# Optimization experiments

Hardware: AMD Instinct MI355X
Metric: run time of the kernel (lower is better)

Reference implementation:

```python
import jax, jax.numpy as jnp
import numpy as np

EPS = 1e-8  # matches torch F.cosine_similarity eps default


def setup_inputs() -> dict:
    key = jax.random.key(0)
    k1, k2 = jax.random.split(key)
    z = jax.random.normal(k1, (8192, 256), dtype=jnp.float32)            # [N, d] node latents
    embedding_weight = jax.random.normal(k2, (4096, 256), dtype=jnp.float32)  # [V, d] codebook
    return {"z": z, "embedding_weight": embedding_weight}


def _l2_normalize(x):
    # torch cosine_similarity clamps each norm at eps before dividing
    n = jnp.sqrt(jnp.sum(x * x, axis=-1, keepdims=True))
    return x / jnp.maximum(n, EPS)


def reference(z, embedding_weight):
    # decode_edges: sigmoid(z @ z^T) -> [N, N]
    adj = jax.nn.sigmoid(jnp.matmul(z, z.T))

    # decode_node_features: cosine similarity of every node latent vs every
    # codebook vector, then argmax over the codebook axis. Instead of the
    # naive [N, V, d] broadcast, normalize both sides and take a single
    # [N, d] x [d, V] matmul -> [N, V], then reduce with argmax.
    zn = _l2_normalize(z)                   # [N, d]
    en = _l2_normalize(embedding_weight)    # [V, d]
    cosine_sim = jnp.matmul(zn, en.T)       # [N, V]
    decoded_indices = jnp.argmax(cosine_sim, axis=1)  # [N] int

    return adj, decoded_indices
```

## Files before the change

### kernel.cpp

```cpp
#include <hip/hip_runtime.h>
#include <stdint.h>
#include <math.h>

#define D_DIM 256
#define NZ 8192
#define NV 4096

typedef __bf16 bf16;
typedef __attribute__((ext_vector_type(8))) __bf16 bf16x8;
typedef __attribute__((ext_vector_type(4))) float f32x4;

__device__ __forceinline__ void stage16(const bf16* g, bf16* lbase) {
#if __has_builtin(__builtin_amdgcn_global_load_lds)
  __builtin_amdgcn_global_load_lds(
      (const __attribute__((address_space(1))) void*)(uintptr_t)g,
      (__attribute__((address_space(3))) void*)(uint32_t)(uintptr_t)lbase,
      16, 0, 0);
#endif
}

__global__ void prep_kernel(const float* __restrict__ z, const float* __restrict__ E,
                            bf16* __restrict__ zh, bf16* __restrict__ zl,
                            bf16* __restrict__ eh, float* __restrict__ rinvZ,
                            float* __restrict__ rinvE,
                            unsigned long long* __restrict__ slots) {
  __shared__ float red[4];
  const int row = blockIdx.x;
  const int t = threadIdx.x;
  const bool isZ = row < NZ;
  const int r = isZ ? row : row - NZ;
  const float* src = isZ ? z : E;
  const float x = src[(size_t)r * D_DIM + t];
  const bf16 h = (bf16)x;
  if (isZ) {
    zh[(size_t)r * D_DIM + t] = h;
    zl[(size_t)r * D_DIM + t] = (bf16)(x - (float)h);
  } else {
    eh[(size_t)r * D_DIM + t] = h;
  }
  float s = x * x;
#pragma unroll
  for (int off = 32; off; off >>= 1) s += __shfl_xor(s, off);
  if ((t & 63) == 0) red[t >> 6] = s;
  __syncthreads();
  if (t == 0) {
    const float tot = red[0] + red[1] + red[2] + red[3];
    const float rv = 1.0f / fmaxf(sqrtf(tot), 1e-8f);
    if (isZ) {
      rinvZ[r] = rv;
      slots[r] = 0ull;
    } else {
      rinvE[r] = rv;
    }
  }
}

__device__ __forceinline__ unsigned long long packvc(float v, int col) {
  const uint32_t b = __float_as_uint(v);
  const uint32_t key = b ^ ((uint32_t)((int32_t)b >> 31) | 0x80000000u);
  return ((unsigned long long)key << 32) | (uint32_t)(~(uint32_t)col);
}

__global__ __launch_bounds__(256, 2) void cos_kernel(
    const bf16* __restrict__ Ah, const bf16* __restrict__ Bh, bf16* __restrict__ Dm,
    const float* __restrict__ rinvZ, const float* __restrict__ rinvE,
    unsigned long long* __restrict__ slots) {
  __shared__ bf16 lAh[128 * 32], lBh[128 * 32];
  const int tid = threadIdx.x;
  const int lane = tid & 63;
  const int w = tid >> 6;
  const int wr = w >> 1, wc = w & 1;
  const int l15 = lane & 15, q = lane >> 4;
  const int bm = blockIdx.y * 128;
  const int bn = blockIdx.x * 128;

  f32x4 acc[4][4] = {};

  for (int kt = 0; kt < 8; ++kt) {
    const int ko = kt * 32;
#pragma unroll
    for (int i = 0; i < 2; ++i) {
      const int c = w * 128 + i * 64 + lane;
      const int r = c >> 2;
      const int kb = (c & 3) << 3;
      const int lofs = (w * 128 + i * 64) * 8;
      stage16(Ah + (size_t)(bm + r) * D_DIM + ko + kb, lAh + lofs);
      stage16(Bh + (size_t)(bn + r) * D_DIM + ko + kb, lBh + lofs);
    }
    __syncthreads();
    bf16x8 fa[4], fb[4];
#pragma unroll
    for (int ms = 0; ms < 4; ++ms)
      fa[ms] = *(const bf16x8*)&lAh[(wr * 64 + ms * 16 + l15) * 32 + q * 8];
#pragma unroll
    for (int ns = 0; ns < 4; ++ns)
      fb[ns] = *(const bf16x8*)&lBh[(wc * 64 + ns * 16 + l15) * 32 + q * 8];
#pragma unroll
    for (int ms = 0; ms < 4; ++ms)
#pragma unroll
      for (int ns = 0; ns < 4; ++ns)
        acc[ms][ns] = __builtin_amdgcn_mfma_f32_16x16x32_bf16(fa[ms], fb[ns], acc[ms][ns], 0, 0, 0);
    __syncthreads();
  }

  float rc[4];
  int cols[4];
#pragma unroll
  for (int ns = 0; ns < 4; ++ns) {
    cols[ns] = bn + wc * 64 + ns * 16 + l15;
    rc[ns] = rinvE[cols[ns]];
  }
#pragma unroll
  for (int ms = 0; ms < 4; ++ms) {
    const int rb = bm + wr * 64 + ms * 16 + q * 4;
#pragma unroll
    for (int r = 0; r < 4; ++r) {
      const int rowg = rb + r;
      const float rr = rinvZ[rowg];
      bf16* drow = Dm + (size_t)rowg * NV;
      unsigned long long best = 0ull;
#pragma unroll
      for (int ns = 0; ns < 4; ++ns) {
        const float v = acc[ms][ns][r] * rc[ns] * rr;
        drow[cols[ns]] = (bf16)v;
        const unsigned long long p = packvc(v, cols[ns]);
        best = p > best ? p : best;
      }
#pragma unroll
      for (int off = 1; off < 16; off <<= 1) {
        const unsigned long long o = __shfl_xor(best, off);
        best = o > best ? o : best;
      }
      if (l15 == 0) atomicMax(&slots[rowg], best);
    }
  }
}

__device__ __forceinline__ int tri_base(int i) { return i * 64 - ((i * (i - 1)) >> 1); }

__global__ __launch_bounds__(256, 2) void adj_kernel(const bf16* __restrict__ Ah,
                                                     const bf16* __restrict__ Al,
                                                     float* __restrict__ out) {
  __shared__ bf16 lAh[128 * 32], lAl[128 * 32], lBh[128 * 32], lBl[128 * 32];
  int k = blockIdx.x;
  k = (k & 7) * 260 + (k >> 3);
  const double disc = 4160.25 - 2.0 * (double)k;
  int bi = (int)(64.5 - sqrt(disc));
  while (tri_base(bi + 1) <= k) ++bi;
  while (tri_base(bi) > k) --bi;
  const int bj = bi + (k - tri_base(bi));
  const int bm = bi * 128, bn = bj * 128;

  const int tid = threadIdx.x;
  const int lane = tid & 63;
  const int w = tid >> 6;
  const int wr = w >> 1, wc = w & 1;
  const int l15 = lane & 15, q = lane >> 4;

  f32x4 acc[4][4] = {};

  for (int kt = 0; kt < 8; ++kt) {
    const int ko = kt * 32;
#pragma unroll
    for (int i = 0; i < 2; ++i) {
      const int c = w * 128 + i * 64 + lane;
      const int r = c >> 2;
      const int kb = (c & 3) << 3;
      const size_t ga = (size_t)(bm + r) * D_DIM + ko + kb;
      const size_t gb = (size_t)(bn + r) * D_DIM + ko + kb;
      const int lofs = (w * 128 + i * 64) * 8;
      stage16(Ah + ga, lAh + lofs);
      stage16(Al + ga, lAl + lofs);
      stage16(Ah + gb, lBh + lofs);
      stage16(Al + gb, lBl + lofs);
    }
    __syncthreads();
    bf16x8 fah[4], fal[4], fbh[4], fbl[4];
#pragma unroll
    for (int ms = 0; ms < 4; ++ms) {
      const int m = wr * 64 + ms * 16 + l15;
      fah[ms] = *(const bf16x8*)&lAh[m * 32 + q * 8];
      fal[ms] = *(const bf16x8*)&lAl[m * 32 + q * 8];
    }
#pragma unroll
    for (int ns = 0; ns < 4; ++ns) {
      const int n = wc * 64 + ns * 16 + l15;
      fbh[ns] = *(const bf16x8*)&lBh[n * 32 + q * 8];
      fbl[ns] = *(const bf16x8*)&lBl[n * 32 + q * 8];
    }
#pragma unroll
    for (int ms = 0; ms < 4; ++ms)
#pragma unroll
      for (int ns = 0; ns < 4; ++ns) {
        acc[ms][ns] = __builtin_amdgcn_mfma_f32_16x16x32_bf16(fah[ms], fbh[ns], acc[ms][ns], 0, 0, 0);
        acc[ms][ns] = __builtin_amdgcn_mfma_f32_16x16x32_bf16(fah[ms], fbl[ns], acc[ms][ns], 0, 0, 0);
        acc[ms][ns] = __builtin_amdgcn_mfma_f32_16x16x32_bf16(fal[ms], fbh[ns], acc[ms][ns], 0, 0, 0);
      }
    __syncthreads();
  }

#pragma unroll
  for (int ms = 0; ms < 4; ++ms)
#pragma unroll
    for (int ns = 0; ns < 4; ++ns)
#pragma unroll
      for (int r = 0; r < 4; ++r)
        acc[ms][ns][r] = __builtin_amdgcn_rcpf(1.0f + __expf(-acc[ms][ns][r]));

#pragma unroll
  for (int ms = 0; ms < 4; ++ms) {
    const int rb = bm + wr * 64 + ms * 16 + q * 4;
#pragma unroll
    for (int r = 0; r < 4; ++r) {
      const size_t ro = (size_t)(rb + r) * NZ;
#pragma unroll
      for (int ns = 0; ns < 4; ++ns) {
        const int col = bn + wc * 64 + ns * 16 + l15;
        out[ro + col] = acc[ms][ns][r];
      }
    }
  }
  if (bi != bj) {
#pragma unroll
    for (int ms = 0; ms < 4; ++ms) {
      const int rb = bm + wr * 64 + ms * 16 + q * 4;
#pragma unroll
      for (int ns = 0; ns < 4; ++ns) {
        const int col = bn + wc * 64 + ns * 16 + l15;
        *(f32x4*)&out[(size_t)col * NZ + rb] = acc[ms][ns];
      }
    }
  }
}

__device__ __forceinline__ double block_reduce(double v, double* red, int t) {
#pragma unroll
  for (int off = 32; off; off >>= 1) v += __shfl_xor(v, off);
  __syncthreads();
  if ((t & 63) == 0) red[t >> 6] = v;
  __syncthreads();
  return red[0] + red[1] + red[2] + red[3];
}

__global__ __launch_bounds__(256) void refine_kernel(
    const bf16* __restrict__ Dm, const unsigned long long* __restrict__ slots,
    const float* __restrict__ z, const float* __restrict__ E,
    float* __restrict__ out_idx) {
  __shared__ int s_cand[128];
  __shared__ int s_cnt;
  __shared__ double s_red[4];
  const int row = blockIdx.x;
  const int t = threadIdx.x;
  if (t == 0) s_cnt = 0;
  __syncthreads();

  const unsigned long long packed = slots[row];
  const uint32_t key = (uint32_t)(packed >> 32);
  const uint32_t fb = (key & 0x80000000u) ? (key ^ 0x80000000u) : ~key;
  const float M = __uint_as_float(fb);
  const float thr = M - 2e-2f;

  const bf16* drow = Dm + (size_t)row * NV;
  for (int c8 = t; c8 < NV / 8; c8 += 256) {
    const bf16x8 v = *(const bf16x8*)(drow + c8 * 8);
#pragma unroll
    for (int j = 0; j < 8; ++j) {
      if ((float)v[j] >= thr) {
        const int kk = atomicAdd(&s_cnt, 1);
        if (kk < 128) s_cand[kk] = c8 * 8 + j;
      }
    }
  }
  __syncthreads();
  const int cnt = s_cnt < 128 ? s_cnt : 128;

  const double zv = (double)z[(size_t)row * D_DIM + t];
  const double sz2 = block_reduce(zv * zv, s_red, t);

  double v1 = -1e30, v2 = -1e30;
  int c1 = 0x7fffffff, c2 = 0x7fffffff;
  for (int i = 0; i < cnt; ++i) {
    const int c = s_cand[i];
    const double ev = (double)E[(size_t)c * D_DIM + t];
    const double dot = block_reduce(zv * ev, s_red, t);
    const double se2 = block_reduce(ev * ev, s_red, t);
    if (t == 0) {
      const double cv = dot / (fmax(sqrt(sz2), 1e-8) * fmax(sqrt(se2), 1e-8));
      if (cv > v1 || (cv == v1 && c < c1)) {
        v2 = v1; c2 = c1; v1 = cv; c1 = c;
      } else if (cv > v2 || (cv == v2 && c < c2)) {
        v2 = cv; c2 = c;
      }
    }
  }
  if (t == 0) {
    int pick = c1;
    if (c2 != 0x7fffffff && (v1 - v2) < 3e-7) pick = c2;
    out_idx[row] = (float)pick;
  }
}

extern "C" void kernel_launch(void* const* d_in, const int* in_sizes, int n_in,
                              void* d_out, int out_size, void* d_ws, size_t ws_size,
                              hipStream_t stream) {
  const float* z = (const float*)d_in[0];
  const float* E = (const float*)d_in[1];
  float* out = (float*)d_out;

  char* ws = (char*)d_ws;
  bf16* zh = (bf16*)ws;
  bf16* zl = zh + (size_t)NZ * D_DIM;
  bf16* eh = zl + (size_t)NZ * D_DIM;
  float* rinvZ = (float*)(eh + (size_t)NV * D_DIM);
  float* rinvE = rinvZ + NZ;
  unsigned long long* slots = (unsigned long long*)(rinvE + NV);

  bf16* Dm = (bf16*)out;
  float* idx_out = out + (size_t)NZ * NZ;

  prep_kernel<<<NZ + NV, 256, 0, stream>>>(z, E, zh, zl, eh, rinvZ, rinvE, slots);

  dim3 g2(NV / 128, NZ / 128);
  cos_kernel<<<g2, 256, 0, stream>>>(zh, eh, Dm, rinvZ, rinvE, slots);

  refine_kernel<<<NZ, 256, 0, stream>>>(Dm, slots, z, E, idx_out);

  adj_kernel<<<2080, 256, 0, stream>>>(zh, zl, out);
}
```

Baseline: 434.2 us.

## Parallelize refine candidates across waves and raise GEMM occupancy to three blocks

The refine kernel now scores candidates with one wave each, using shuffle reductions, instead of running two block-wide reductions with barriers per candidate. It also narrows the candidate threshold, which cuts how many candidates get rescored. Both GEMM kernels now load A fragments per row-subtile inside the loop, which lowers register pressure, and their launch bounds rise to three blocks per SIMD to allow more occupancy. The tighter threshold risks missing the true argmax when bf16 rounding error is large, and the new launch bound may cause register spills.

After: 393.9 us. -9.3%, faster.

```diff
diff --git a/kernel.cpp b/kernel.cpp
--- a/kernel.cpp
+++ b/kernel.cpp
@@ -61,7 +61,7 @@
   return ((unsigned long long)key << 32) | (uint32_t)(~(uint32_t)col);
 }
 
-__global__ __launch_bounds__(256, 2) void cos_kernel(
+__global__ __launch_bounds__(256, 3) void cos_kernel(
     const bf16* __restrict__ Ah, const bf16* __restrict__ Bh, bf16* __restrict__ Dm,
     const float* __restrict__ rinvZ, const float* __restrict__ rinvE,
     unsigned long long* __restrict__ slots) {
@@ -88,18 +88,17 @@
       stage16(Bh + (size_t)(bn + r) * D_DIM + ko + kb, lBh + lofs);
     }
     __syncthreads();
-    bf16x8 fa[4], fb[4];
-#pragma unroll
-    for (int ms = 0; ms < 4; ++ms)
-      fa[ms] = *(const bf16x8*)&lAh[(wr * 64 + ms * 16 + l15) * 32 + q * 8];
+    bf16x8 fb[4];
 #pragma unroll
     for (int ns = 0; ns < 4; ++ns)
       fb[ns] = *(const bf16x8*)&lBh[(wc * 64 + ns * 16 + l15) * 32 + q * 8];
 #pragma unroll
-    for (int ms = 0; ms < 4; ++ms)
+    for (int ms = 0; ms < 4; ++ms) {
+      const bf16x8 fa = *(const bf16x8*)&lAh[(wr * 64 + ms * 16 + l15) * 32 + q * 8];
 #pragma unroll
       for (int ns = 0; ns < 4; ++ns)
-        acc[ms][ns] = __builtin_amdgcn_mfma_f32_16x16x32_bf16(fa[ms], fb[ns], acc[ms][ns], 0, 0, 0);
+        acc[ms][ns] = __builtin_amdgcn_mfma_f32_16x16x32_bf16(fa, fb[ns], acc[ms][ns], 0, 0, 0);
+    }
     __syncthreads();
   }
 
@@ -138,7 +137,7 @@
 
 __device__ __forceinline__ int tri_base(int i) { return i * 64 - ((i * (i - 1)) >> 1); }
 
-__global__ __launch_bounds__(256, 2) void adj_kernel(const bf16* __restrict__ Ah,
+__global__ __launch_bounds__(256, 3) void adj_kernel(const bf16* __restrict__ Ah,
                                                      const bf16* __restrict__ Al,
                                                      float* __restrict__ out) {
   __shared__ bf16 lAh[128 * 32], lAl[128 * 32], lBh[128 * 32], lBl[128 * 32];
@@ -175,13 +174,7 @@
       stage16(Al + gb, lBl + lofs);
     }
     __syncthreads();
-    bf16x8 fah[4], fal[4], fbh[4], fbl[4];
-#pragma unroll
-    for (int ms = 0; ms < 4; ++ms) {
-      const int m = wr * 64 + ms * 16 + l15;
-      fah[ms] = *(const bf16x8*)&lAh[m * 32 + q * 8];
-      fal[ms] = *(const bf16x8*)&lAl[m * 32 + q * 8];
-    }
+    bf16x8 fbh[4], fbl[4];
 #pragma unroll
     for (int ns = 0; ns < 4; ++ns) {
       const int n = wc * 64 + ns * 16 + l15;
@@ -189,13 +182,17 @@
       fbl[ns] = *(const bf16x8*)&lBl[n * 32 + q * 8];
     }
 #pragma unroll
-    for (int ms = 0; ms < 4; ++ms)
+    for (int ms = 0; ms < 4; ++ms) {
+      const int m = wr * 64 + ms * 16 + l15;
+      const bf16x8 fah = *(const bf16x8*)&lAh[m * 32 + q * 8];
+      const bf16x8 fal = *(const bf16x8*)&lAl[m * 32 + q * 8];
 #pragma unroll
       for (int ns = 0; ns < 4; ++ns) {
-        acc[ms][ns] = __builtin_amdgcn_mfma_f32_16x16x32_bf16(fah[ms], fbh[ns], acc[ms][ns], 0, 0, 0);
-        acc[ms][ns] = __builtin_amdgcn_mfma_f32_16x16x32_bf16(fah[ms], fbl[ns], acc[ms][ns], 0, 0, 0);
-        acc[ms][ns] = __builtin_amdgcn_mfma_f32_16x16x32_bf16(fal[ms], fbh[ns], acc[ms][ns], 0, 0, 0);
-      }
+        acc[ms][ns] = __builtin_amdgcn_mfma_f32_16x16x32_bf16(fah, fbh[ns], acc[ms][ns], 0, 0, 0);
+        acc[ms][ns] = __builtin_amdgcn_mfma_f32_16x16x32_bf16(fah, fbl[ns], acc[ms][ns], 0, 0, 0);
+        acc[ms][ns] = __builtin_amdgcn_mfma_f32_16x16x32_bf16(fal, fbh[ns], acc[ms][ns], 0, 0, 0);
+      }
+    }
     __syncthreads();
   }
 
@@ -231,15 +228,6 @@
       }
     }
   }
-}
-
-__device__ __forceinline__ double block_reduce(double v, double* red, int t) {
-#pragma unroll
-  for (int off = 32; off; off >>= 1) v += __shfl_xor(v, off);
-  __syncthreads();
-  if ((t & 63) == 0) red[t >> 6] = v;
-  __syncthreads();
-  return red[0] + red[1] + red[2] + red[3];
 }
 
 __global__ __launch_bounds__(256) void refine_kernel(
@@ -248,9 +236,13 @@
     float* __restrict__ out_idx) {
   __shared__ int s_cand[128];
   __shared__ int s_cnt;
-  __shared__ double s_red[4];
+  __shared__ double s_dot[128];
+  __shared__ double s_se2[128];
+  __shared__ double s_sz2;
   const int row = blockIdx.x;
   const int t = threadIdx.x;
+  const int lane = t & 63;
+  const int w = t >> 6;
   if (t == 0) s_cnt = 0;
   __syncthreads();
 
@@ -258,7 +250,7 @@
   const uint32_t key = (uint32_t)(packed >> 32);
   const uint32_t fb = (key & 0x80000000u) ? (key ^ 0x80000000u) : ~key;
   const float M = __uint_as_float(fb);
-  const float thr = M - 2e-2f;
+  const float thr = M - 1.2e-2f;
 
   const bf16* drow = Dm + (size_t)row * NV;
   for (int c8 = t; c8 < NV / 8; c8 += 256) {
@@ -274,26 +266,51 @@
   __syncthreads();
   const int cnt = s_cnt < 128 ? s_cnt : 128;
 
-  const double zv = (double)z[(size_t)row * D_DIM + t];
-  const double sz2 = block_reduce(zv * zv, s_red, t);
-
-  double v1 = -1e30, v2 = -1e30;
-  int c1 = 0x7fffffff, c2 = 0x7fffffff;
-  for (int i = 0; i < cnt; ++i) {
+  double zr[4];
+#pragma unroll
+  for (int j = 0; j < 4; ++j) zr[j] = (double)z[(size_t)row * D_DIM + lane + 64 * j];
+
+  if (w == 0) {
+    double s = zr[0] * zr[0] + zr[1] * zr[1] + zr[2] * zr[2] + zr[3] * zr[3];
+#pragma unroll
+    for (int off = 32; off; off >>= 1) s += __shfl_xor(s, off);
+    if (lane == 0) s_sz2 = s;
+  }
+
+  for (int i = w; i < cnt; i += 4) {
     const int c = s_cand[i];
-    const double ev = (double)E[(size_t)c * D_DIM + t];
-    const double dot = block_reduce(zv * ev, s_red, t);
-    const double se2 = block_reduce(ev * ev, s_red, t);
-    if (t == 0) {
-      const double cv = dot / (fmax(sqrt(sz2), 1e-8) * fmax(sqrt(se2), 1e-8));
+    double d = 0.0, e2 = 0.0;
+#pragma unroll
+    for (int j = 0; j < 4; ++j) {
+      const double ev = (double)E[(size_t)c * D_DIM + lane + 64 * j];
+      d += zr[j] * ev;
+      e2 += ev * ev;
+    }
+#pragma unroll
+    for (int off = 32; off; off >>= 1) {
+      d += __shfl_xor(d, off);
+      e2 += __shfl_xor(e2, off);
+    }
+    if (lane == 0) {
+      s_dot[i] = d;
+      s_se2[i] = e2;
+    }
+  }
+  __syncthreads();
+
+  if (t == 0) {
+    const double sz = fmax(sqrt(s_sz2), 1e-8);
+    double v1 = -1e30, v2 = -1e30;
+    int c1 = 0x7fffffff, c2 = 0x7fffffff;
+    for (int i = 0; i < cnt; ++i) {
+      const int c = s_cand[i];
+      const double cv = s_dot[i] / (sz * fmax(sqrt(s_se2[i]), 1e-8));
       if (cv > v1 || (cv == v1 && c < c1)) {
         v2 = v1; c2 = c1; v1 = cv; c1 = c;
       } else if (cv > v2 || (cv == v2 && c < c2)) {
         v2 = cv; c2 = c;
       }
     }
-  }
-  if (t == 0) {
     int pick = c1;
     if (c2 != 0x7fffffff && (v1 - v2) < 3e-7) pick = c2;
     out_idx[row] = (float)pick;
```
